# Kernel optimization log

Measured on AMD Instinct MI355X. Metric: run time of the kernel, lower is better.

The kernel has to match this reference:

```python
import jax, jax.numpy as jnp
import numpy as np

H = 8        # heads
DH = 64      # dim_head
K = 16       # num_neighbors
EMB = 512    # emb_dim
INNER = H * DH
AINNER = 4 * DH  # per-head attn_mlp hidden width
POSH = 64


def setup_inputs() -> dict:
    key = jax.random.key(0)
    ks = jax.random.split(key, 20)
    bs, n = 2, 1024
    rn = lambda k, s, sc=1.0: jax.random.normal(k, s, jnp.float32) * sc
    return {
        "query": rn(ks[0], (bs, n, EMB)),
        "key_in": rn(ks[1], (bs, n, EMB)),
        "value": rn(ks[2], (bs, n, EMB)),
        "canonical": rn(ks[3], (bs, n, 3)),
        "w_q": rn(ks[4], (EMB, INNER), EMB ** -0.5),
        "w_k": rn(ks[5], (EMB, INNER), EMB ** -0.5),
        "w_v": rn(ks[6], (EMB, INNER), EMB ** -0.5),
        "w_out": rn(ks[7], (INNER, EMB), INNER ** -0.5),
        "b_out": rn(ks[8], (EMB,), 0.02),
        "pos_w1": rn(ks[9], (3, POSH), 3 ** -0.5),
        "pos_b1": rn(ks[10], (POSH,), 0.02),
        "pos_w2": rn(ks[11], (POSH, INNER), POSH ** -0.5),
        "pos_b2": rn(ks[12], (INNER,), 0.02),
        "aw1": rn(ks[13], (H, AINNER, DH), DH ** -0.5),   # grouped conv1 weight per head: (out=4*DH, in=DH)
        "ab1": rn(ks[14], (H, AINNER), 0.02),
        "aw2": rn(ks[15], (H, DH, AINNER), AINNER ** -0.5),  # grouped conv2: (out=DH, in=4*DH)
        "ab2": rn(ks[16], (H, DH), 0.02),
    }


def reference(query, key_in, value, canonical, w_q, w_k, w_v, w_out, b_out,
              pos_w1, pos_b1, pos_w2, pos_b2, aw1, ab1, aw2, ab2):
    bs, n, _ = query.shape
    # projections, then b n (h d) -> b h n d
    to_heads = lambda t: t.reshape(bs, n, H, DH).transpose(0, 2, 1, 3)
    q = to_heads(query @ w_q)
    k = to_heads(key_in @ w_k)
    v = to_heads(value @ w_v)

    # KNN on canonical coords: (b,n,n) squared distances, k smallest (includes self)
    d2 = jnp.sum((canonical[:, :, None, :] - canonical[:, None, :, :]) ** 2, axis=-1)
    _, nbr = jax.lax.top_k(-d2, K)                       # (b,n,K)
    idx = (nbr + (jnp.arange(bs) * n)[:, None, None]).reshape(-1)  # flat rows into bs*n

    # relative position embedding
    pos_nn = canonical.reshape(bs * n, 3)[idx].reshape(bs, n, K, 3)
    rel = pos_nn - canonical[:, :, None, :]
    rpe = jax.nn.relu(rel @ pos_w1 + pos_b1) @ pos_w2 + pos_b2        # (b,n,K,inner)
    rpe = rpe.reshape(bs, n, K, H, DH).transpose(0, 3, 1, 2, 4)       # (b,h,i,j,d)

    # faithful replication of the original view(bs*n,-1)[idx] gathers on (b,h,n,d) tensors
    gather = lambda t: t.reshape(bs * n, -1)[idx].reshape(bs, H, n, K, DH)
    qg, kg, vg = gather(q), gather(k), gather(v)
    vg = vg + rpe
    x = (qg - kg) + rpe                                  # (b,h,i,j,d)

    # grouped 1x1 conv attn_mlp == per-head MLP over d
    hdn = jax.nn.relu(jnp.einsum('bhijd,hed->bhije', x, aw1) + ab1[None, :, None, None, :])
    sim = jnp.einsum('bhije,hde->bhijd', hdn, aw2) + ab2[None, :, None, None, :]

    attn = jax.nn.softmax(sim, axis=3)                   # softmax over neighbors j
    norm = jnp.sqrt(jnp.sum(attn * attn, axis=2, keepdims=True))  # F.normalize over i
    attn = attn / jnp.maximum(norm, 1e-12)

    agg = jnp.einsum('bhijd,bhijd->bhid', attn, vg)      # (b,h,i,d)
    agg = agg.transpose(0, 2, 1, 3).reshape(bs, n, INNER)
    return agg @ w_out + b_out
```

## Files before the change

kernel.cpp:

```cpp
#include <hip/hip_runtime.h>


#define BS 2
#define NPT 1024
#define HH 8
#define DH 64
#define KNN 16
#define EMB 512
#define INNER 512
#define AINNER 256
#define POSH 64

typedef unsigned short u16;
typedef unsigned int u32;
typedef __attribute__((ext_vector_type(8))) short bf16x8;
typedef __attribute__((ext_vector_type(4))) float f32x4;

__device__ __forceinline__ float bf2f(u16 b) { union { u32 u; float f; } v; v.u = ((u32)b) << 16; return v.f; }
__device__ __forceinline__ u16 f2bf_rne(float f) {
    u32 x = __float_as_uint(f);
    u32 r = x + 0x7fffu + ((x >> 16) & 1u);
    return (u16)(r >> 16);
}
__device__ __forceinline__ void split2(float f, u16& hi, u16& lo) {
    u32 bits = __float_as_uint(f);
    hi = (u16)(bits >> 16);
    float resid = f - __uint_as_float(bits & 0xffff0000u);
    lo = (u16)(__float_as_uint(resid) >> 16);
}
__device__ __forceinline__ void split4(float4 f, ushort4& h, ushort4& l) {
    split2(f.x, h.x, l.x); split2(f.y, h.y, l.y);
    split2(f.z, h.z, l.z); split2(f.w, h.w, l.w);
}

__global__ __launch_bounds__(256) void k_preT(const float* __restrict__ aw1,
                                              const float* __restrict__ aw2,
                                              const float* __restrict__ pw2,
                                              const float* __restrict__ wq,
                                              const float* __restrict__ wk,
                                              const float* __restrict__ wv,
                                              const float* __restrict__ wout,
                                              u16* __restrict__ w1hi, u16* __restrict__ w2hi,
                                              u16* __restrict__ rw2hi,
                                              u16* __restrict__ o0h, u16* __restrict__ o0l,
                                              u16* __restrict__ o1h, u16* __restrict__ o1l,
                                              u16* __restrict__ o2h, u16* __restrict__ o2l,
                                              u16* __restrict__ o3h, u16* __restrict__ o3l)
{
    __shared__ float S[64][65];
    const int bx = blockIdx.x, t = threadIdx.x;
    if (bx < 1152) {
        int idx = bx * 256 + t;
        if (idx < 131072) {
            w1hi[idx] = f2bf_rne(aw1[idx]);
        } else if (idx < 262144) {
            int k2 = idx - 131072;
            w2hi[k2] = f2bf_rne(aw2[k2]);
        } else {
            int k2 = idx - 262144;
            int p = k2 & 63; int hd = k2 >> 6;
            int h = hd >> 6; int d = hd & 63;
            rw2hi[k2] = f2bf_rne(pw2[(size_t)p * INNER + h * DH + d]);
        }
        return;
    }
    const int v0 = bx - 1152;
    const int e0 = (v0 & 7) * 64, c0 = ((v0 >> 3) & 7) * 64, z = v0 >> 6;
    const float* src; u16* dh; u16* dl;
    switch (z) {
        case 0:  src = wq;   dh = o0h; dl = o0l; break;
        case 1:  src = wk;   dh = o1h; dl = o1l; break;
        case 2:  src = wv;   dh = o2h; dl = o2l; break;
        default: src = wout; dh = o3h; dl = o3l; break;
    }
    #pragma unroll
    for (int s = 0; s < 16; ++s) {
        int v = s * 256 + t; int r = v >> 6, c = v & 63;
        S[r][c] = src[(size_t)(e0 + r) * 512 + c0 + c];
    }
    __syncthreads();
    #pragma unroll
    for (int s = 0; s < 16; ++s) {
        int v = s * 256 + t; int c = v >> 6, e = v & 63;
        u16 hi, lo; split2(S[e][c], hi, lo);
        size_t off = (size_t)(c0 + c) * 512 + e0 + e;
        dh[off] = hi; dl[off] = lo;
    }
}

__global__ __launch_bounds__(256) void k_projM(const float* __restrict__ qf,
                                               const float* __restrict__ kf,
                                               const float* __restrict__ vf,
                                               const u16* __restrict__ wqh, const u16* __restrict__ wql,
                                               const u16* __restrict__ wkh, const u16* __restrict__ wkl,
                                               const u16* __restrict__ wvh, const u16* __restrict__ wvl,
                                               float* __restrict__ Dws, float* __restrict__ Vws)
{
    __shared__ u16 S[12][64 * 40];
    const int t = threadIdx.x, l = t & 63, w = t >> 6;
    const int lm = l & 15, lg = (l >> 4) * 8;
    const int g0 = blockIdx.x * 64, c0 = blockIdx.y * 64;
    const int sr = t >> 2, sc = (t & 3) * 8;

    f32x4 accD[4] = {{0,0,0,0},{0,0,0,0},{0,0,0,0},{0,0,0,0}};
    f32x4 accV[4] = {{0,0,0,0},{0,0,0,0},{0,0,0,0},{0,0,0,0}};

    for (int ks = 0; ks < 16; ++ks) {
        const int k0 = ks * 32;
        if (ks) __syncthreads();
        #pragma unroll
        for (int m = 0; m < 3; ++m) {
            const float* sp = (m == 0 ? qf : (m == 1 ? kf : vf))
                              + (size_t)(g0 + sr) * 512 + k0 + sc;
            float4 f0 = *(const float4*)sp;
            float4 f1 = *(const float4*)(sp + 4);
            if (m == 1) {
                f0.x = -f0.x; f0.y = -f0.y; f0.z = -f0.z; f0.w = -f0.w;
                f1.x = -f1.x; f1.y = -f1.y; f1.z = -f1.z; f1.w = -f1.w;
            }
            ushort4 h0, l0, h1, l1;
            split4(f0, h0, l0); split4(f1, h1, l1);
            *(ushort4*)&S[2*m  ][sr * 40 + sc]     = h0;
            *(ushort4*)&S[2*m  ][sr * 40 + sc + 4] = h1;
            *(ushort4*)&S[2*m+1][sr * 40 + sc]     = l0;
            *(ushort4*)&S[2*m+1][sr * 40 + sc + 4] = l1;
        }
        #define STG(p, base) \
            *(uint4*)&S[p][sr * 40 + sc] = *(const uint4*)&(base)[(size_t)(c0 + sr) * 512 + k0 + sc];
        STG(6, wqh) STG(7, wql) STG(8, wkh) STG(9, wkl) STG(10, wvh) STG(11, wvl)
        #undef STG
        __syncthreads();

        const int ao = (w * 16 + lm) * 40 + lg;
        bf16x8 aqh = *(const bf16x8*)&S[0][ao];
        bf16x8 aql = *(const bf16x8*)&S[1][ao];
        bf16x8 akh = *(const bf16x8*)&S[2][ao];
        bf16x8 akl = *(const bf16x8*)&S[3][ao];
        bf16x8 avh = *(const bf16x8*)&S[4][ao];
        bf16x8 avl = *(const bf16x8*)&S[5][ao];
        #pragma unroll
        for (int ct = 0; ct < 4; ++ct) {
            const int bo = (ct * 16 + lm) * 40 + lg;
            bf16x8 bqh = *(const bf16x8*)&S[6][bo];
            bf16x8 bql = *(const bf16x8*)&S[7][bo];
            bf16x8 bkh = *(const bf16x8*)&S[8][bo];
            bf16x8 bkl = *(const bf16x8*)&S[9][bo];
            bf16x8 bvh = *(const bf16x8*)&S[10][bo];
            bf16x8 bvl = *(const bf16x8*)&S[11][bo];
            accD[ct] = __builtin_amdgcn_mfma_f32_16x16x32_bf16(aqh, bqh, accD[ct], 0, 0, 0);
            accD[ct] = __builtin_amdgcn_mfma_f32_16x16x32_bf16(aql, bqh, accD[ct], 0, 0, 0);
            accD[ct] = __builtin_amdgcn_mfma_f32_16x16x32_bf16(aqh, bql, accD[ct], 0, 0, 0);
            accD[ct] = __builtin_amdgcn_mfma_f32_16x16x32_bf16(akh, bkh, accD[ct], 0, 0, 0);
            accD[ct] = __builtin_amdgcn_mfma_f32_16x16x32_bf16(akl, bkh, accD[ct], 0, 0, 0);
            accD[ct] = __builtin_amdgcn_mfma_f32_16x16x32_bf16(akh, bkl, accD[ct], 0, 0, 0);
            accV[ct] = __builtin_amdgcn_mfma_f32_16x16x32_bf16(avh, bvh, accV[ct], 0, 0, 0);
            accV[ct] = __builtin_amdgcn_mfma_f32_16x16x32_bf16(avl, bvh, accV[ct], 0, 0, 0);
            accV[ct] = __builtin_amdgcn_mfma_f32_16x16x32_bf16(avh, bvl, accV[ct], 0, 0, 0);
        }
    }

    const int b = blockIdx.x >> 4;
    const int h = blockIdx.y;
    #pragma unroll
    for (int ct = 0; ct < 4; ++ct) {
        #pragma unroll
        for (int r = 0; r < 4; ++r) {
            int g = g0 + w * 16 + (l >> 4) * 4 + r;
            int i = g & 1023;
            size_t off = (((size_t)(b * HH + h)) * NPT + i) * DH + ct * 16 + lm;
            Dws[off] = accD[ct][r];
            Vws[off] = accV[ct][r];
        }
    }
}

__global__ __launch_bounds__(256) void k_knn(const float* __restrict__ canonical,
                                             const float* __restrict__ pw1,
                                             const float* __restrict__ pb1,
                                             int* __restrict__ nbr,
                                             u16* __restrict__ h1g)
{
    const int t = threadIdx.x, l = t & 63, w = t >> 6;
    const int i = blockIdx.x * 4 + w;
    const int b = blockIdx.y;
    const float* cb = canonical + (size_t)b * NPT * 3;
    const float qx = cb[i*3+0], qy = cb[i*3+1], qz = cb[i*3+2];
    float d2v[16];
    #pragma unroll
    for (int k = 0; k < 16; ++k) {
        int j = l * 16 + k;
        float dx = __fsub_rn(cb[j*3+0], qx);
        float dy = __fsub_rn(cb[j*3+1], qy);
        float dz = __fsub_rn(cb[j*3+2], qz);
        d2v[k] = __fadd_rn(__fadd_rn(__fmul_rn(dx,dx), __fmul_rn(dy,dy)), __fmul_rn(dz,dz));
    }
    unsigned alive = 0xFFFFu;
    int js[16];
    int* out = nbr + ((size_t)b * NPT + i) * KNN;
    #pragma unroll
    for (int sel = 0; sel < KNN; ++sel) {
        float bv = __builtin_inff(); int bk = 16;
        #pragma unroll
        for (int k = 0; k < 16; ++k) {
            float v = ((alive >> k) & 1u) ? d2v[k] : __builtin_inff();
            if (v < bv) { bv = v; bk = k; }
        }
        int bj = l * 16 + bk;
        #pragma unroll
        for (int m = 32; m >= 1; m >>= 1) {
            float ov = __shfl_xor(bv, m, 64);
            int   oj = __shfl_xor(bj, m, 64);
            if (ov < bv || (ov == bv && oj < bj)) { bv = ov; bj = oj; }
        }
        if (l == 0) out[sel] = bj;
        js[sel] = bj;
        if ((bj >> 4) == l) alive &= ~(1u << (bj & 15));
    }
    const float pw10 = pw1[l], pw11 = pw1[64 + l], pw12 = pw1[128 + l], pb1v = pb1[l];
    u16* hrow = h1g + (((size_t)b * NPT + i) * KNN) * 64 + l;
    #pragma unroll
    for (int j = 0; j < KNN; ++j) {
        int nv = js[j];
        float rx = cb[nv*3+0] - qx;
        float ry = cb[nv*3+1] - qy;
        float rz = cb[nv*3+2] - qz;
        float a = pb1v;
        a = fmaf(rx, pw10, a);
        a = fmaf(ry, pw11, a);
        a = fmaf(rz, pw12, a);
        hrow[j * 64] = f2bf_rne(fmaxf(a, 0.0f));
    }
}

__global__ __launch_bounds__(256, 3) void k_attn(const float* __restrict__ Dws,
                                              const float* __restrict__ Vws,
                                              const int* __restrict__ nbr,
                                              const float* __restrict__ pb2,
                                              const float* __restrict__ ab1,
                                              const float* __restrict__ ab2,
                                              const u16* __restrict__ w1hi,
                                              const u16* __restrict__ w2hi,
                                              const u16* __restrict__ rw2hi,
                                              const u16* __restrict__ h1g,
                                              u16* __restrict__ prodb,
                                              float* __restrict__ npart2)
{
    const int it = blockIdx.x, h = blockIdx.y, b = blockIdx.z, t = threadIdx.x;
    const int l = t & 63, w = t >> 6;
    const int lm = l & 15, lg = (l >> 4) * 8;
    const int dd = w * 16 + lm;

    __shared__ u16 Xs[2][16 * 72];
    __shared__ u16 Hs[2][16 * 264];
    __shared__ u16 rw2s[64 * 72];
    __shared__ int nbrrow[KNN];

    bf16x8 w1f[8], w2f[8];
    float b1v[4];
    #pragma unroll
    for (int q = 0; q < 4; ++q) {
        int e = (w * 4 + q) * 16 + lm;
        b1v[q] = ab1[h * AINNER + e];
        #pragma unroll
        for (int kc = 0; kc < 2; ++kc)
            w1f[q*2+kc] = *(const bf16x8*)&w1hi[((size_t)(h * AINNER + e)) * DH + kc * 32 + lg];
    }
    const float b2v  = ab2[h * DH + dd];
    const float pb2v = pb2[h * DH + dd];
    #pragma unroll
    for (int kc = 0; kc < 8; ++kc)
        w2f[kc] = *(const bf16x8*)&w2hi[((size_t)(h * DH + dd)) * AINNER + kc * 32 + lg];

    for (int v = t; v < 64 * 64; v += 256) {
        int d = v >> 6, p = v & 63;
        rw2s[d * 72 + p] = rw2hi[(h * DH + d) * POSH + p];
    }
    if (t < KNN) nbrrow[t] = nbr[((size_t)b * NPT + h * 128 + it) * KNN + t];
    __syncthreads();

    float dvp[2][4], vwp[2][4];
    bf16x8 h1f[2][2];
    auto gather = [&](int pp) {
        #pragma unroll
        for (int u = 0; u < 2; ++u) {
            const int ti = 2 * pp + u;
            const int i = it * 8 + ti;
            #pragma unroll
            for (int r = 0; r < 4; ++r) {
                int j = (l >> 4) * 4 + r;
                int nv = nbrrow[2 * ti + (j >> 3)];
                size_t off = (((size_t)b * HH + (nv >> 7)) * NPT + (nv & 127) * 8 + (j & 7)) * DH + dd;
                dvp[u][r] = Dws[off];
                vwp[u][r] = Vws[off];
            }
            const u16* hb = h1g + (((size_t)b * NPT + i) * KNN + lm) * 64;
            h1f[u][0] = *(const bf16x8*)&hb[lg];
            h1f[u][1] = *(const bf16x8*)&hb[32 + lg];
        }
    };
    gather(0);

    float npacc[4] = {0.f, 0.f, 0.f, 0.f};
    float vvreg[2][4];

    for (int p = 0; p < 4; ++p) {
        #pragma unroll
        for (int u = 0; u < 2; ++u) {
            f32x4 racc = {0.f, 0.f, 0.f, 0.f};
            #pragma unroll
            for (int kc = 0; kc < 2; ++kc) {
                bf16x8 rb = *(const bf16x8*)&rw2s[dd * 72 + kc * 32 + lg];
                racc = __builtin_amdgcn_mfma_f32_16x16x32_bf16(h1f[u][kc], rb, racc, 0, 0, 0);
            }
            #pragma unroll
            for (int r = 0; r < 4; ++r) {
                int j = (l >> 4) * 4 + r;
                float rp = racc[r] + pb2v;
                Xs[u][j * 72 + dd] = f2bf_rne(dvp[u][r] + rp);
                vvreg[u][r] = vwp[u][r] + rp;
            }
        }
        if (p < 3) gather(p + 1);
        __syncthreads();
        #pragma unroll
        for (int u = 0; u < 2; ++u) {
            f32x4 acc1[4] = {{0,0,0,0},{0,0,0,0},{0,0,0,0},{0,0,0,0}};
            #pragma unroll
            for (int kc = 0; kc < 2; ++kc) {
                bf16x8 ah = *(const bf16x8*)&Xs[u][lm * 72 + kc * 32 + lg];
                #pragma unroll
                for (int q = 0; q < 4; ++q)
                    acc1[q] = __builtin_amdgcn_mfma_f32_16x16x32_bf16(ah, w1f[q*2+kc], acc1[q], 0, 0, 0);
            }
            #pragma unroll
            for (int q = 0; q < 4; ++q) {
                int ee = (w * 4 + q) * 16 + lm;
                #pragma unroll
                for (int r = 0; r < 4; ++r) {
                    int jj = (l >> 4) * 4 + r;
                    Hs[u][jj * 264 + ee] = f2bf_rne(fmaxf(acc1[q][r] + b1v[q], 0.0f));
                }
            }
        }
        __syncthreads();
        #pragma unroll
        for (int u = 0; u < 2; ++u) {
            const int i = it * 8 + 2 * p + u;
            f32x4 acc2[4] = {{0,0,0,0},{0,0,0,0},{0,0,0,0},{0,0,0,0}};
            #pragma unroll
            for (int kc = 0; kc < 8; ++kc) {
                bf16x8 ah = *(const bf16x8*)&Hs[u][lm * 264 + kc * 32 + lg];
                acc2[kc & 3] = __builtin_amdgcn_mfma_f32_16x16x32_bf16(ah, w2f[kc], acc2[kc & 3], 0, 0, 0);
            }
            float sim[4];
            #pragma unroll
            for (int r = 0; r < 4; ++r)
                sim[r] = ((acc2[0][r] + acc2[1][r]) + (acc2[2][r] + acc2[3][r])) + b2v;
            float m = fmaxf(fmaxf(sim[0], sim[1]), fmaxf(sim[2], sim[3]));
            m = fmaxf(m, __shfl_xor(m, 16, 64));
            m = fmaxf(m, __shfl_xor(m, 32, 64));
            float ex[4], s = 0.0f;
            #pragma unroll
            for (int r = 0; r < 4; ++r) { ex[r] = __expf(sim[r] - m); s += ex[r]; }
            s += __shfl_xor(s, 16, 64);
            s += __shfl_xor(s, 32, 64);
            float inv = 1.0f / s;
            u16* po = prodb + (((size_t)(b * HH + h) * NPT + i) * KNN) * DH + dd;
            #pragma unroll
            for (int r = 0; r < 4; ++r) {
                float af = ex[r] * inv;
                po[((l >> 4) * 4 + r) * DH] = f2bf_rne(af * vvreg[u][r]);
                npacc[r] = fmaf(af, af, npacc[r]);
            }
        }
    }

    float* np = npart2 + ((size_t)((b * HH + h) * 128 + it)) * 1024 + ((l >> 4) * 4) * 64 + dd;
    #pragma unroll
    for (int r = 0; r < 4; ++r) np[r * 64] = npacc[r];
}

__global__ __launch_bounds__(256) void k_normR(const float* __restrict__ npart2, float* __restrict__ nrm)
{
    __shared__ float red[256];
    const int vout = blockIdx.x * 64 + (threadIdx.x & 63);
    const int chunk = threadIdx.x >> 6;
    const int bh = vout >> 10, jd = vout & 1023;
    const float* src = npart2 + (size_t)bh * 131072 + jd + (size_t)chunk * 32768;
    float s = 0.0f;
    #pragma unroll 4
    for (int k = 0; k < 32; ++k) s += src[k * 1024];
    red[threadIdx.x] = s;
    __syncthreads();
    if (chunk == 0) {
        float tot = (red[threadIdx.x] + red[threadIdx.x + 64])
                  + (red[threadIdx.x + 128] + red[threadIdx.x + 192]);
        nrm[vout] = sqrtf(tot);
    }
}

__global__ __launch_bounds__(256) void k_agg(const u16* __restrict__ prodb,
                                             const float* __restrict__ nrm,
                                             u16* __restrict__ agghi,
                                             u16* __restrict__ agglo)
{
    const int it = blockIdx.x, h = blockIdx.y, b = blockIdx.z, t = threadIdx.x;
    const int l = t & 63, w = t >> 6;
    const int i = it * 4 + w;
    __shared__ float rn[KNN * DH];
    for (int v = t; v < KNN * DH; v += 256)
        rn[v] = 1.0f / fmaxf(nrm[(size_t)(b * HH + h) * 1024 + v], 1e-12f);
    __syncthreads();
    const size_t row = ((size_t)(b * HH + h) * NPT + i) * (KNN * DH);
    bf16x8 p0 = *(const bf16x8*)&prodb[row + l * 8];
    bf16x8 p1 = *(const bf16x8*)&prodb[row + 512 + l * 8];
    const int dbase = (l & 7) * 8;
    float4 ra = *(const float4*)&rn[(l >> 3) * 64 + dbase];
    float4 rb = *(const float4*)&rn[(l >> 3) * 64 + dbase + 4];
    float4 rc = *(const float4*)&rn[(8 + (l >> 3)) * 64 + dbase];
    float4 rd = *(const float4*)&rn[(8 + (l >> 3)) * 64 + dbase + 4];
    const float r0[8] = {ra.x, ra.y, ra.z, ra.w, rb.x, rb.y, rb.z, rb.w};
    const float r1[8] = {rc.x, rc.y, rc.z, rc.w, rd.x, rd.y, rd.z, rd.w};
    float acc[8];
    #pragma unroll
    for (int e = 0; e < 8; ++e)
        acc[e] = bf2f((u16)p0[e]) * r0[e] + bf2f((u16)p1[e]) * r1[e];
    #pragma unroll
    for (int mask = 8; mask <= 32; mask <<= 1)
        #pragma unroll
        for (int e = 0; e < 8; ++e)
            acc[e] += __shfl_xor(acc[e], mask, 64);
    if (l < 8) {
        size_t off = ((size_t)b * NPT + i) * INNER + h * DH + l * 8;
        ushort4 h0, l0, h1, l1;
        split2(acc[0], h0.x, l0.x); split2(acc[1], h0.y, l0.y);
        split2(acc[2], h0.z, l0.z); split2(acc[3], h0.w, l0.w);
        split2(acc[4], h1.x, l1.x); split2(acc[5], h1.y, l1.y);
        split2(acc[6], h1.z, l1.z); split2(acc[7], h1.w, l1.w);
        *(ushort4*)&agghi[off]     = h0;
        *(ushort4*)&agghi[off + 4] = h1;
        *(ushort4*)&agglo[off]     = l0;
        *(ushort4*)&agglo[off + 4] = l1;
    }
}

__global__ __launch_bounds__(256) void k_outM(const u16* __restrict__ agghi, const u16* __restrict__ agglo,
                                              const u16* __restrict__ wth, const u16* __restrict__ wtl,
                                              const float* __restrict__ bout,
                                              float* __restrict__ outp)
{
    __shared__ u16 S[4][64 * 40];
    const int t = threadIdx.x, l = t & 63, w = t >> 6;
    const int lm = l & 15, lg = (l >> 4) * 8;
    const int g0 = blockIdx.x * 64, c0 = blockIdx.y * 64;
    const int sr = t >> 2, sc = (t & 3) * 8;

    f32x4 acc[4] = {{0,0,0,0},{0,0,0,0},{0,0,0,0},{0,0,0,0}};
    float bv4[4];
    #pragma unroll
    for (int ct = 0; ct < 4; ++ct) bv4[ct] = bout[c0 + ct * 16 + lm];

    for (int ks = 0; ks < 16; ++ks) {
        const int k0 = ks * 32;
        if (ks) __syncthreads();
        *(uint4*)&S[0][sr * 40 + sc] = *(const uint4*)&agghi[(size_t)(g0 + sr) * 512 + k0 + sc];
        *(uint4*)&S[1][sr * 40 + sc] = *(const uint4*)&agglo[(size_t)(g0 + sr) * 512 + k0 + sc];
        *(uint4*)&S[2][sr * 40 + sc] = *(const uint4*)&wth[(size_t)(c0 + sr) * 512 + k0 + sc];
        *(uint4*)&S[3][sr * 40 + sc] = *(const uint4*)&wtl[(size_t)(c0 + sr) * 512 + k0 + sc];
        __syncthreads();

        const int ao = (w * 16 + lm) * 40 + lg;
        bf16x8 ah = *(const bf16x8*)&S[0][ao];
        bf16x8 al = *(const bf16x8*)&S[1][ao];
        #pragma unroll
        for (int ct = 0; ct < 4; ++ct) {
            const int bo = (ct * 16 + lm) * 40 + lg;
            bf16x8 bh = *(const bf16x8*)&S[2][bo];
            bf16x8 bl = *(const bf16x8*)&S[3][bo];
            acc[ct] = __builtin_amdgcn_mfma_f32_16x16x32_bf16(ah, bh, acc[ct], 0, 0, 0);
            acc[ct] = __builtin_amdgcn_mfma_f32_16x16x32_bf16(al, bh, acc[ct], 0, 0, 0);
            acc[ct] = __builtin_amdgcn_mfma_f32_16x16x32_bf16(ah, bl, acc[ct], 0, 0, 0);
        }
    }
    #pragma unroll
    for (int ct = 0; ct < 4; ++ct) {
        #pragma unroll
        for (int r = 0; r < 4; ++r) {
            int g = g0 + w * 16 + (l >> 4) * 4 + r;
            outp[(size_t)g * 512 + c0 + ct * 16 + lm] = acc[ct][r] + bv4[ct];
        }
    }
}

extern "C" void kernel_launch(void* const* d_in, const int* in_sizes, int n_in,
                              void* d_out, int out_size, void* d_ws, size_t ws_size,
                              hipStream_t stream) {
    const float* query     = (const float*)d_in[0];
    const float* key_in    = (const float*)d_in[1];
    const float* value     = (const float*)d_in[2];
    const float* canonical = (const float*)d_in[3];
    const float* wq   = (const float*)d_in[4];
    const float* wk   = (const float*)d_in[5];
    const float* wv   = (const float*)d_in[6];
    const float* wout = (const float*)d_in[7];
    const float* bout = (const float*)d_in[8];
    const float* pw1  = (const float*)d_in[9];
    const float* pb1  = (const float*)d_in[10];
    const float* pw2  = (const float*)d_in[11];
    const float* pb2  = (const float*)d_in[12];
    const float* aw1  = (const float*)d_in[13];
    const float* ab1  = (const float*)d_in[14];
    const float* aw2  = (const float*)d_in[15];
    const float* ab2  = (const float*)d_in[16];

    float* ws    = (float*)d_ws;
    float* Dws   = ws;
    float* Vws   = ws + 1048576;
    float* aggp  = ws + 2097152;
    float* nrm   = ws + 3162112;
    int*   nbr   = (int*)(ws + 3293184);
    float* attnR = ws + 3325952;

    u16* agghi = (u16*)aggp;
    u16* agglo = agghi + 1048576;

    u16* prodb = (u16*)attnR;
    u16* pl   = (u16*)(attnR + 8388608);
    u16* wqTh = pl;                u16* wqTl = pl + 262144;
    u16* wkTh = pl + 524288;       u16* wkTl = pl + 786432;
    u16* wvTh = pl + 1048576;      u16* wvTl = pl + 1310720;
    float* npart2 = attnR + 12582912;
    u16* h1g = (u16*)(attnR + 14680064);

    u16* u16b  = (u16*)(ws + 20103168);
    u16* w1hi  = u16b;
    u16* w2hi  = u16b + 262144;
    u16* rw2hi = u16b + 524288;
    u16* wouTh = u16b + 17367040;
    u16* wouTl = u16b + 17629184;

    k_preT<<<1408, 256, 0, stream>>>(aw1, aw2, pw2, wq, wk, wv, wout,
                                     w1hi, w2hi, rw2hi,
                                     wqTh, wqTl, wkTh, wkTl, wvTh, wvTl, wouTh, wouTl);
    k_knn<<<dim3(256, BS), 256, 0, stream>>>(canonical, pw1, pb1, nbr, h1g);
    k_projM<<<dim3(32, 8), 256, 0, stream>>>(query, key_in, value,
                                             wqTh, wqTl, wkTh, wkTl, wvTh, wvTl, Dws, Vws);
    k_attn<<<dim3(128, HH, BS), 256, 0, stream>>>(Dws, Vws, nbr, pb2, ab1, ab2,
                                                  w1hi, w2hi, rw2hi, h1g, prodb, npart2);
    k_normR<<<256, 256, 0, stream>>>(npart2, nrm);
    k_agg<<<dim3(256, HH, BS), 256, 0, stream>>>(prodb, nrm, agghi, agglo);
    k_outM<<<dim3(32, 8), 256, 0, stream>>>(agghi, agglo, wouTh, wouTl, bout, (float*)d_out);
}
```

Measured before the change: 141.4 us.

## Merge KNN into weight-prep kernel and double per-block rows in attn and agg

The KNN/positional-hidden computation now runs as extra blocks inside the weight-preparation kernel, which removes one kernel launch and lets the two independent jobs share the GPU. The attention kernel handles 16 query rows per block instead of 8. That halves the grid and amortizes the per-block loading of per-head weights into shared memory, and the norm-partial reduction shrinks to match. The aggregation kernel also processes 16 rows per block, reusing the reciprocal-norm table it loads. The cost is fewer blocks, so less parallelism and possibly worse latency hiding in the attention kernel.

```diff
diff --git a/kernel.cpp b/kernel.cpp
--- a/kernel.cpp
+++ b/kernel.cpp
@@ -40,12 +40,17 @@
                                               const float* __restrict__ wk,
                                               const float* __restrict__ wv,
                                               const float* __restrict__ wout,
+                                              const float* __restrict__ canonical,
+                                              const float* __restrict__ pw1,
+                                              const float* __restrict__ pb1,
                                               u16* __restrict__ w1hi, u16* __restrict__ w2hi,
                                               u16* __restrict__ rw2hi,
                                               u16* __restrict__ o0h, u16* __restrict__ o0l,
                                               u16* __restrict__ o1h, u16* __restrict__ o1l,
                                               u16* __restrict__ o2h, u16* __restrict__ o2l,
-                                              u16* __restrict__ o3h, u16* __restrict__ o3l)
+                                              u16* __restrict__ o3h, u16* __restrict__ o3l,
+                                              int* __restrict__ nbr,
+                                              u16* __restrict__ h1g)
 {
     __shared__ float S[64][65];
     const int bx = blockIdx.x, t = threadIdx.x;
@@ -64,27 +69,83 @@
         }
         return;
     }
-    const int v0 = bx - 1152;
-    const int e0 = (v0 & 7) * 64, c0 = ((v0 >> 3) & 7) * 64, z = v0 >> 6;
-    const float* src; u16* dh; u16* dl;
-    switch (z) {
-        case 0:  src = wq;   dh = o0h; dl = o0l; break;
-        case 1:  src = wk;   dh = o1h; dl = o1l; break;
-        case 2:  src = wv;   dh = o2h; dl = o2l; break;
-        default: src = wout; dh = o3h; dl = o3l; break;
-    }
-    #pragma unroll
-    for (int s = 0; s < 16; ++s) {
-        int v = s * 256 + t; int r = v >> 6, c = v & 63;
-        S[r][c] = src[(size_t)(e0 + r) * 512 + c0 + c];
-    }
-    __syncthreads();
-    #pragma unroll
-    for (int s = 0; s < 16; ++s) {
-        int v = s * 256 + t; int c = v >> 6, e = v & 63;
-        u16 hi, lo; split2(S[e][c], hi, lo);
-        size_t off = (size_t)(c0 + c) * 512 + e0 + e;
-        dh[off] = hi; dl[off] = lo;
+    if (bx < 1408) {
+        const int v0 = bx - 1152;
+        const int e0 = (v0 & 7) * 64, c0 = ((v0 >> 3) & 7) * 64, z = v0 >> 6;
+        const float* src; u16* dh; u16* dl;
+        switch (z) {
+            case 0:  src = wq;   dh = o0h; dl = o0l; break;
+            case 1:  src = wk;   dh = o1h; dl = o1l; break;
+            case 2:  src = wv;   dh = o2h; dl = o2l; break;
+            default: src = wout; dh = o3h; dl = o3l; break;
+        }
+        #pragma unroll
+        for (int s = 0; s < 16; ++s) {
+            int v = s * 256 + t; int r = v >> 6, c = v & 63;
+            S[r][c] = src[(size_t)(e0 + r) * 512 + c0 + c];
+        }
+        __syncthreads();
+        #pragma unroll
+        for (int s = 0; s < 16; ++s) {
+            int v = s * 256 + t; int c = v >> 6, e = v & 63;
+            u16 hi, lo; split2(S[e][c], hi, lo);
+            size_t off = (size_t)(c0 + c) * 512 + e0 + e;
+            dh[off] = hi; dl[off] = lo;
+        }
+        return;
+    }
+    {
+        const int v0 = bx - 1408;
+        const int b = v0 >> 8, xb = v0 & 255;
+        const int l = t & 63, w = t >> 6;
+        const int i = xb * 4 + w;
+        const float* cb = canonical + (size_t)b * NPT * 3;
+        const float qx = cb[i*3+0], qy = cb[i*3+1], qz = cb[i*3+2];
+        float d2v[16];
+        #pragma unroll
+        for (int k = 0; k < 16; ++k) {
+            int j = l * 16 + k;
+            float dx = __fsub_rn(cb[j*3+0], qx);
+            float dy = __fsub_rn(cb[j*3+1], qy);
+            float dz = __fsub_rn(cb[j*3+2], qz);
+            d2v[k] = __fadd_rn(__fadd_rn(__fmul_rn(dx,dx), __fmul_rn(dy,dy)), __fmul_rn(dz,dz));
+        }
+        unsigned alive = 0xFFFFu;
+        int js[16];
+        int* out = nbr + ((size_t)b * NPT + i) * KNN;
+        #pragma unroll
+        for (int sel = 0; sel < KNN; ++sel) {
+            float bv = __builtin_inff(); int bk = 16;
+            #pragma unroll
+            for (int k = 0; k < 16; ++k) {
+                float v = ((alive >> k) & 1u) ? d2v[k] : __builtin_inff();
+                if (v < bv) { bv = v; bk = k; }
+            }
+            int bj = l * 16 + bk;
+            #pragma unroll
+            for (int m = 32; m >= 1; m >>= 1) {
+                float ov = __shfl_xor(bv, m, 64);
+                int   oj = __shfl_xor(bj, m, 64);
+                if (ov < bv || (ov == bv && oj < bj)) { bv = ov; bj = oj; }
+            }
+            if (l == 0) out[sel] = bj;
+            js[sel] = bj;
+            if ((bj >> 4) == l) alive &= ~(1u << (bj & 15));
+        }
+        const float pw10 = pw1[l], pw11 = pw1[64 + l], pw12 = pw1[128 + l], pb1v = pb1[l];
+        u16* hrow = h1g + (((size_t)b * NPT + i) * KNN) * 64 + l;
+        #pragma unroll
+        for (int j = 0; j < KNN; ++j) {
+            int nv = js[j];
+            float rx = cb[nv*3+0] - qx;
+            float ry = cb[nv*3+1] - qy;
+            float rz = cb[nv*3+2] - qz;
+            float a = pb1v;
+            a = fmaf(rx, pw10, a);
+            a = fmaf(ry, pw11, a);
+            a = fmaf(rz, pw12, a);
+            hrow[j * 64] = f2bf_rne(fmaxf(a, 0.0f));
+        }
     }
 }
 
@@ -174,64 +235,6 @@
     }
 }
 
-__global__ __launch_bounds__(256) void k_knn(const float* __restrict__ canonical,
-                                             const float* __restrict__ pw1,
-                                             const float* __restrict__ pb1,
-                                             int* __restrict__ nbr,
-                                             u16* __restrict__ h1g)
-{
-    const int t = threadIdx.x, l = t & 63, w = t >> 6;
-    const int i = blockIdx.x * 4 + w;
-    const int b = blockIdx.y;
-    const float* cb = canonical + (size_t)b * NPT * 3;
-    const float qx = cb[i*3+0], qy = cb[i*3+1], qz = cb[i*3+2];
-    float d2v[16];
-    #pragma unroll
-    for (int k = 0; k < 16; ++k) {
-        int j = l * 16 + k;
-        float dx = __fsub_rn(cb[j*3+0], qx);
-        float dy = __fsub_rn(cb[j*3+1], qy);
-        float dz = __fsub_rn(cb[j*3+2], qz);
-        d2v[k] = __fadd_rn(__fadd_rn(__fmul_rn(dx,dx), __fmul_rn(dy,dy)), __fmul_rn(dz,dz));
-    }
-    unsigned alive = 0xFFFFu;
-    int js[16];
-    int* out = nbr + ((size_t)b * NPT + i) * KNN;
-    #pragma unroll
-    for (int sel = 0; sel < KNN; ++sel) {
-        float bv = __builtin_inff(); int bk = 16;
-        #pragma unroll
-        for (int k = 0; k < 16; ++k) {
-            float v = ((alive >> k) & 1u) ? d2v[k] : __builtin_inff();
-            if (v < bv) { bv = v; bk = k; }
-        }
-        int bj = l * 16 + bk;
-        #pragma unroll
-        for (int m = 32; m >= 1; m >>= 1) {
-            float ov = __shfl_xor(bv, m, 64);
-            int   oj = __shfl_xor(bj, m, 64);
-            if (ov < bv || (ov == bv && oj < bj)) { bv = ov; bj = oj; }
-        }
-        if (l == 0) out[sel] = bj;
-        js[sel] = bj;
-        if ((bj >> 4) == l) alive &= ~(1u << (bj & 15));
-    }
-    const float pw10 = pw1[l], pw11 = pw1[64 + l], pw12 = pw1[128 + l], pb1v = pb1[l];
-    u16* hrow = h1g + (((size_t)b * NPT + i) * KNN) * 64 + l;
-    #pragma unroll
-    for (int j = 0; j < KNN; ++j) {
-        int nv = js[j];
-        float rx = cb[nv*3+0] - qx;
-        float ry = cb[nv*3+1] - qy;
-        float rz = cb[nv*3+2] - qz;
-        float a = pb1v;
-        a = fmaf(rx, pw10, a);
-        a = fmaf(ry, pw11, a);
-        a = fmaf(rz, pw12, a);
-        hrow[j * 64] = f2bf_rne(fmaxf(a, 0.0f));
-    }
-}
-
 __global__ __launch_bounds__(256, 3) void k_attn(const float* __restrict__ Dws,
                                               const float* __restrict__ Vws,
                                               const int* __restrict__ nbr,
@@ -253,7 +256,7 @@
     __shared__ u16 Xs[2][16 * 72];
     __shared__ u16 Hs[2][16 * 264];
     __shared__ u16 rw2s[64 * 72];
-    __shared__ int nbrrow[KNN];
+    __shared__ int nbrrow[2 * KNN];
 
     bf16x8 w1f[8], w2f[8];
     float b1v[4];
@@ -275,7 +278,8 @@
         int d = v >> 6, p = v & 63;
         rw2s[d * 72 + p] = rw2hi[(h * DH + d) * POSH + p];
     }
-    if (t < KNN) nbrrow[t] = nbr[((size_t)b * NPT + h * 128 + it) * KNN + t];
+    if (t < 2 * KNN)
+        nbrrow[t] = nbr[((size_t)b * NPT + h * 128 + it * 2 + (t >> 4)) * KNN + (t & 15)];
     __syncthreads();
 
     float dvp[2][4], vwp[2][4];
@@ -284,11 +288,11 @@
         #pragma unroll
         for (int u = 0; u < 2; ++u) {
             const int ti = 2 * pp + u;
-            const int i = it * 8 + ti;
+            const int i = it * 16 + ti;
             #pragma unroll
             for (int r = 0; r < 4; ++r) {
                 int j = (l >> 4) * 4 + r;
-                int nv = nbrrow[2 * ti + (j >> 3)];
+                int nv = nbrrow[((ti >> 3) << 4) + 2 * (ti & 7) + (j >> 3)];
                 size_t off = (((size_t)b * HH + (nv >> 7)) * NPT + (nv & 127) * 8 + (j & 7)) * DH + dd;
                 dvp[u][r] = Dws[off];
                 vwp[u][r] = Vws[off];
@@ -303,7 +307,7 @@
     float npacc[4] = {0.f, 0.f, 0.f, 0.f};
     float vvreg[2][4];
 
-    for (int p = 0; p < 4; ++p) {
+    for (int p = 0; p < 8; ++p) {
         #pragma unroll
         for (int u = 0; u < 2; ++u) {
             f32x4 racc = {0.f, 0.f, 0.f, 0.f};
@@ -320,7 +324,7 @@
                 vvreg[u][r] = vwp[u][r] + rp;
             }
         }
-        if (p < 3) gather(p + 1);
+        if (p < 7) gather(p + 1);
         __syncthreads();
         #pragma unroll
         for (int u = 0; u < 2; ++u) {
@@ -345,7 +349,7 @@
         __syncthreads();
         #pragma unroll
         for (int u = 0; u < 2; ++u) {
-            const int i = it * 8 + 2 * p + u;
+            const int i = it * 16 + 2 * p + u;
             f32x4 acc2[4] = {{0,0,0,0},{0,0,0,0},{0,0,0,0},{0,0,0,0}};
             #pragma unroll
             for (int kc = 0; kc < 8; ++kc) {
@@ -375,7 +379,7 @@
         }
     }
 
-    float* np = npart2 + ((size_t)((b * HH + h) * 128 + it)) * 1024 + ((l >> 4) * 4) * 64 + dd;
+    float* np = npart2 + ((size_t)((b * HH + h) * 64 + it)) * 1024 + ((l >> 4) * 4) * 64 + dd;
     #pragma unroll
     for (int r = 0; r < 4; ++r) np[r * 64] = npacc[r];
 }
@@ -386,10 +390,10 @@
     const int vout = blockIdx.x * 64 + (threadIdx.x & 63);
     const int chunk = threadIdx.x >> 6;
     const int bh = vout >> 10, jd = vout & 1023;
-    const float* src = npart2 + (size_t)bh * 131072 + jd + (size_t)chunk * 32768;
+    const float* src = npart2 + (size_t)bh * 65536 + jd + (size_t)chunk * 16384;
     float s = 0.0f;
     #pragma unroll 4
-    for (int k = 0; k < 32; ++k) s += src[k * 1024];
+    for (int k = 0; k < 16; ++k) s += src[k * 1024];
     red[threadIdx.x] = s;
     __syncthreads();
     if (chunk == 0) {
@@ -406,14 +410,10 @@
 {
     const int it = blockIdx.x, h = blockIdx.y, b = blockIdx.z, t = threadIdx.x;
     const int l = t & 63, w = t >> 6;
-    const int i = it * 4 + w;
     __shared__ float rn[KNN * DH];
     for (int v = t; v < KNN * DH; v += 256)
         rn[v] = 1.0f / fmaxf(nrm[(size_t)(b * HH + h) * 1024 + v], 1e-12f);
     __syncthreads();
-    const size_t row = ((size_t)(b * HH + h) * NPT + i) * (KNN * DH);
-    bf16x8 p0 = *(const bf16x8*)&prodb[row + l * 8];
-    bf16x8 p1 = *(const bf16x8*)&prodb[row + 512 + l * 8];
     const int dbase = (l & 7) * 8;
     float4 ra = *(const float4*)&rn[(l >> 3) * 64 + dbase];
     float4 rb = *(const float4*)&rn[(l >> 3) * 64 + dbase + 4];
@@ -421,26 +421,32 @@
     float4 rd = *(const float4*)&rn[(8 + (l >> 3)) * 64 + dbase + 4];
     const float r0[8] = {ra.x, ra.y, ra.z, ra.w, rb.x, rb.y, rb.z, rb.w};
     const float r1[8] = {rc.x, rc.y, rc.z, rc.w, rd.x, rd.y, rd.z, rd.w};
-    float acc[8];
-    #pragma unroll
-    for (int e = 0; e < 8; ++e)
-        acc[e] = bf2f((u16)p0[e]) * r0[e] + bf2f((u16)p1[e]) * r1[e];
-    #pragma unroll
-    for (int mask = 8; mask <= 32; mask <<= 1)
+    for (int g4 = 0; g4 < 4; ++g4) {
+        const int i = it * 16 + g4 * 4 + w;
+        const size_t row = ((size_t)(b * HH + h) * NPT + i) * (KNN * DH);
+        bf16x8 p0 = *(const bf16x8*)&prodb[row + l * 8];
+        bf16x8 p1 = *(const bf16x8*)&prodb[row + 512 + l * 8];
+        float acc[8];
         #pragma unroll
         for (int e = 0; e < 8; ++e)
-            acc[e] += __shfl_xor(acc[e], mask, 64);
-    if (l < 8) {
-        size_t off = ((size_t)b * NPT + i) * INNER + h * DH + l * 8;
-        ushort4 h0, l0, h1, l1;
-        split2(acc[0], h0.x, l0.x); split2(acc[1], h0.y, l0.y);
-        split2(acc[2], h0.z, l0.z); split2(acc[3], h0.w, l0.w);
-        split2(acc[4], h1.x, l1.x); split2(acc[5], h1.y, l1.y);
-        split2(acc[6], h1.z, l1.z); split2(acc[7], h1.w, l1.w);
-        *(ushort4*)&agghi[off]     = h0;
-        *(ushort4*)&agghi[off + 4] = h1;
-        *(ushort4*)&agglo[off]     = l0;
-        *(ushort4*)&agglo[off + 4] = l1;
+            acc[e] = bf2f((u16)p0[e]) * r0[e] + bf2f((u16)p1[e]) * r1[e];
+        #pragma unroll
+        for (int mask = 8; mask <= 32; mask <<= 1)
+            #pragma unroll
+            for (int e = 0; e < 8; ++e)
+                acc[e] += __shfl_xor(acc[e], mask, 64);
+        if (l < 8) {
+            size_t off = ((size_t)b * NPT + i) * INNER + h * DH + l * 8;
+            ushort4 h0, l0, h1, l1;
+            split2(acc[0], h0.x, l0.x); split2(acc[1], h0.y, l0.y);
+            split2(acc[2], h0.z, l0.z); split2(acc[3], h0.w, l0.w);
+            split2(acc[4], h1.x, l1.x); split2(acc[5], h1.y, l1.y);
+            split2(acc[6], h1.z, l1.z); split2(acc[7], h1.w, l1.w);
+            *(ushort4*)&agghi[off]     = h0;
+            *(ushort4*)&agghi[off + 4] = h1;
+            *(ushort4*)&agglo[off]     = l0;
+            *(ushort4*)&agglo[off + 4] = l1;
+        }
     }
 }
 
@@ -539,15 +545,16 @@
     u16* wouTh = u16b + 17367040;
     u16* wouTl = u16b + 17629184;
 
-    k_preT<<<1408, 256, 0, stream>>>(aw1, aw2, pw2, wq, wk, wv, wout,
+    k_preT<<<1920, 256, 0, stream>>>(aw1, aw2, pw2, wq, wk, wv, wout,
+                                     canonical, pw1, pb1,
                                      w1hi, w2hi, rw2hi,
-                                     wqTh, wqTl, wkTh, wkTl, wvTh, wvTl, wouTh, wouTl);
-    k_knn<<<dim3(256, BS), 256, 0, stream>>>(canonical, pw1, pb1, nbr, h1g);
+                                     wqTh, wqTl, wkTh, wkTl, wvTh, wvTl, wouTh, wouTl,
+                                     nbr, h1g);
     k_projM<<<dim3(32, 8), 256, 0, stream>>>(query, key_in, value,
                                              wqTh, wqTl, wkTh, wkTl, wvTh, wvTl, Dws, Vws);
-    k_attn<<<dim3(128, HH, BS), 256, 0, stream>>>(Dws, Vws, nbr, pb2, ab1, ab2,
-                                                  w1hi, w2hi, rw2hi, h1g, prodb, npart2);
+    k_attn<<<dim3(64, HH, BS), 256, 0, stream>>>(Dws, Vws, nbr, pb2, ab1, ab2,
+                                                 w1hi, w2hi, rw2hi, h1g, prodb, npart2);
     k_normR<<<256, 256, 0, stream>>>(npart2, nrm);
-    k_agg<<<dim3(256, HH, BS), 256, 0, stream>>>(prodb, nrm, agghi, agglo);
+    k_agg<<<dim3(64, HH, BS), 256, 0, stream>>>(prodb, nrm, agghi, agglo);
     k_outM<<<dim3(32, 8), 256, 0, stream>>>(agghi, agglo, wouTh, wouTl, bout, (float*)d_out);
 }
```

Measured after the change: 142.4 us. No clear change (+0.7%).
